# Kernel tuning notes

Measured on AMD Instinct MI355X. Metric: run time of the kernel, lower is better.

The kernel has to match this reference:

```python
import jax, jax.numpy as jnp
import numpy as np

N = 8_388_608        # cohort size (2^23)
T_MAX = 1_000_000    # distinct time values -> ~8 ties per unique time


def setup_inputs() -> dict:
    key = jax.random.key(0)
    k1, k2, k3 = jax.random.split(key, 3)
    x = jax.random.normal(k1, (N,), dtype=jnp.float32)  # risk scores
    times = jax.random.randint(k2, (N,), 0, T_MAX).astype(jnp.float32)
    events = (jax.random.uniform(k3, (N,)) < 0.7).astype(jnp.float32)
    target = jnp.stack([times, events], axis=1)  # [N, 2] = [time, event]
    return {"input": x, "target": target}


def _cox_breslow_sqrt_loss(x, target):
    times = target[:, 0]
    events_all = target[:, 1]
    n = x.shape[0]
    # Sort by descending time (risk set = prefix in this ordering).
    sort_idx = jnp.argsort(-times)
    t = times[sort_idx]
    ev = events_all[sort_idx]
    xs = x[sort_idx]
    # Stable prefix log-sum-exp over the risk set.
    log_cum = jax.lax.cumlogsumexp(xs)
    # end_idx[i] = last index of the tie group containing i (groups are
    # contiguous after sorting). Reverse running-min over positions of
    # group-last elements.
    is_last = jnp.concatenate([t[:-1] != t[1:], jnp.ones((1,), dtype=bool)])
    pos = jnp.where(is_last, jnp.arange(n), n)
    end_idx = jnp.flip(jax.lax.cummin(jnp.flip(pos)))
    # Breslow: -sum(x*ev) + sum_groups logcum[group_end] * (#events in group)
    #        == -sum((x - logcum[end_idx]) * ev)
    loss = -jnp.sum((xs - log_cum[end_idx]) * ev)
    # reduction='mean' -> sqrt(loss / n)
    return jnp.sqrt(loss / n)


def reference(input, target):
    return _cox_breslow_sqrt_loss(input, target)
```

## Files before the change

### kernel.cpp

```cpp
#include <hip/hip_runtime.h>
#include <math.h>

#define TMAX 1000000
#define BINW 4096
#define BINSHIFT 12
#define NBIN 245
#define PADN (NBIN * BINW)
#define TILE 8192
#define NTHR 512
#define CAP 36864
#define CURSOR_STRIDE 16
#define BT_STRIDE 8
#define FIXSCALE 65536.0f
#define INV_FIXSCALE (1.0 / 65536.0)

#define OFF_SCAL     0
#define OFF_DONE     16
#define OFF_CURSOR   64
#define OFF_BINTOT   15744
#define OFF_PAYLOAD  31488
#define MEMSET_BYTES 31424
#define NEED_FULL    ((size_t)OFF_PAYLOAD + (size_t)NBIN * CAP * 4)
#define FB_BINTOT    15744
#define FB_CEXCL     17792
#define FB_BEXP      31488
#define FB_BEV       (FB_BEXP + PADN * 4)
#define NEED_MIN     ((size_t)FB_BEV + PADN * 4)

__device__ __forceinline__ int clamp_tau(float t) {
    int tau = (int)t;
    if (tau < 0) tau = 0;
    if (tau >= TMAX) tau = TMAX - 1;
    return tau;
}

__device__ __forceinline__ unsigned enc_payload(float xv, float tv, float ev_f, int* bin_out) {
    int tau = clamp_tau(tv);
    *bin_out = tau >> BINSHIFT;
    int fine = tau & (BINW - 1);
    float ex = __expf(xv);
    unsigned bb = __float_as_uint(ex);
    bb = (bb + 0x7FFFu + ((bb >> 16) & 1u)) >> 16;
    unsigned ev = (ev_f != 0.0f) ? 1u : 0u;
    return (bb << 16) | ((unsigned)fine << 1) | ev;
}

__device__ __forceinline__ float dec_exp(unsigned p) {
    return __uint_as_float((p >> 16) << 16);
}

__device__ __forceinline__ void hist1(unsigned long long* hist, unsigned p) {
    float ex = dec_exp(p);
    unsigned fx = __float2uint_rn(ex * FIXSCALE);
    unsigned long long add = ((unsigned long long)(p & 1u) << 48) | (unsigned long long)fx;
    atomicAdd(&hist[(p >> 1) & (BINW - 1)], add);
}

__device__ __forceinline__ void hist4(unsigned long long* hist, uint4 pv) {
    hist1(hist, pv.x); hist1(hist, pv.y); hist1(hist, pv.z); hist1(hist, pv.w);
}

__global__ __launch_bounds__(NTHR, 8) void k_scatter(const float* __restrict__ x,
                                                     const float* __restrict__ tgt,
                                                     unsigned* __restrict__ cursor,
                                                     unsigned* __restrict__ payload,
                                                     double* __restrict__ bintot,
                                                     double* __restrict__ evx_out, int n) {
    __shared__ unsigned cnt[256];
    __shared__ unsigned lpre[256];
    __shared__ unsigned pay_lds[TILE];
    __shared__ unsigned char binof2[TILE / 2];
    __shared__ unsigned wtot_s[8];
    __shared__ double wpart[8];
    const int t = threadIdx.x;
    const int lane = t & 63;
    const int wv = t >> 6;
    if (t < 256) cnt[t] = 0;
    __syncthreads();

    const int tile0 = blockIdx.x * TILE;
    const int tilecount = min(TILE, n - tile0);
    unsigned pay[16], meta[16];
    double evx = 0.0;

    if (tilecount == TILE) {
        const float4* x4 = (const float4*)x;
        const float4* t4 = (const float4*)tgt;
        const int g0 = blockIdx.x * (TILE / 4);
#pragma unroll
        for (int j = 0; j < 4; ++j) {
            const int g = g0 + j * NTHR + t;
            float4 xv = x4[g];
            float4 ta = t4[2 * g];
            float4 tb = t4[2 * g + 1];
            float xs[4] = {xv.x, xv.y, xv.z, xv.w};
            float ts[4] = {ta.x, ta.z, tb.x, tb.z};
            float es[4] = {ta.y, ta.w, tb.y, tb.w};
#pragma unroll
            for (int e = 0; e < 4; ++e) {
                int bin;
                unsigned p = enc_payload(xs[e], ts[e], es[e], &bin);
                unsigned r = atomicAdd(&cnt[bin], 1u);
                pay[4 * j + e] = p;
                meta[4 * j + e] = ((unsigned)bin << 13) | r;
                if (p & 1) evx += (double)xs[e];
            }
        }
    } else {
        const float2* tg2 = (const float2*)tgt;
#pragma unroll
        for (int j = 0; j < 16; ++j) {
            int idx = tile0 + j * NTHR + t;
            if (idx < n) {
                float xv = x[idx];
                float2 te = tg2[idx];
                int bin;
                unsigned p = enc_payload(xv, te.x, te.y, &bin);
                unsigned r = atomicAdd(&cnt[bin], 1u);
                pay[j] = p;
                meta[j] = ((unsigned)bin << 13) | r;
                if (p & 1) evx += (double)xv;
            } else {
                meta[j] = 0xFFFFFFFFu;
            }
        }
    }
    __syncthreads();

    const unsigned c = (t < 256) ? cnt[t] : 0u;
    unsigned pfx = c;
#pragma unroll
    for (int d = 1; d < 64; d <<= 1) {
        unsigned u = __shfl_up(pfx, d);
        if (lane >= d) pfx += u;
    }
    if (lane == 63) wtot_s[wv] = pfx;
    __syncthreads();
    unsigned wbase = 0;
    if (t < 256) {
        for (int w = 0; w < wv; ++w) wbase += wtot_s[w];
    }
    const unsigned excl = (t < 256) ? (wbase + pfx - c) : 0u;
    if (t < 256) lpre[t] = excl;

    if (t < NBIN && c) cnt[t] = atomicAdd(&cursor[t * CURSOR_STRIDE], c);

    if (t < NBIN && c) {
        for (unsigned j = (excl + 1) >> 1; 2 * j < excl + c; ++j)
            binof2[j] = (unsigned char)t;
    }
    __syncthreads();

#pragma unroll
    for (int j = 0; j < 16; ++j) {
        if (meta[j] != 0xFFFFFFFFu) {
            unsigned bin = meta[j] >> 13;
            pay_lds[lpre[bin] + (meta[j] & 0x1FFFu)] = pay[j];
        }
    }
    __syncthreads();

    if (t < NBIN && c) {
        float s = 0.0f;
        for (unsigned k = excl; k < excl + c; ++k) s += dec_exp(pay_lds[k]);
        unsafeAtomicAdd(&bintot[t * BT_STRIDE], (double)s);
    }

    for (int k = t; k < tilecount; k += NTHR) {
        unsigned b = binof2[(unsigned)k >> 1];
        if (t & 1) {
            while ((unsigned)k >= lpre[b + 1]) ++b;
        }
        unsigned pos = cnt[b] + ((unsigned)k - lpre[b]);
        if (pos < CAP) payload[(size_t)b * CAP + pos] = pay_lds[k];
    }

#pragma unroll
    for (int d = 32; d > 0; d >>= 1) {
        double u = __shfl_down(evx, d);
        if (lane + d < 64) evx += u;
    }
    if (lane == 0) wpart[wv] = evx;
    __syncthreads();
    if (t == 0) {
        double s = 0.0;
        for (int w = 0; w < 8; ++w) s += wpart[w];
        atomicAdd(evx_out, s);
    }
}

__global__ __launch_bounds__(1024) void k_fused(const unsigned* __restrict__ payload,
                                                const unsigned* __restrict__ cursor,
                                                const double* __restrict__ bintot,
                                                double* __restrict__ scal,
                                                unsigned* __restrict__ done,
                                                float* __restrict__ out, int n) {
    __shared__ unsigned long long hist[BINW];
    __shared__ double wsumA[16];
    __shared__ double wsum[16];
    __shared__ double bcast;
    const int b = blockIdx.x;
    const int t = threadIdx.x;
    const int lane = t & 63;
    const int wv = t >> 6;

#pragma unroll
    for (int j = 0; j < BINW / 1024; ++j) hist[t + j * 1024] = 0ull;
    __syncthreads();

    unsigned cnt = cursor[b * CURSOR_STRIDE];
    if (cnt > CAP) cnt = CAP;
    const unsigned* seg = payload + (size_t)b * CAP;
    const uint4* seg4 = (const uint4*)seg;
    const unsigned n4 = cnt >> 2;
    unsigned i = t;
    for (; i + 1024 < n4; i += 2048) {
        uint4 a = seg4[i];
        uint4 c4 = seg4[i + 1024];
        hist4(hist, a);
        hist4(hist, c4);
    }
    for (; i < n4; i += 1024) hist4(hist, seg4[i]);
    for (unsigned k = (n4 << 2) + t; k < cnt; k += 1024) hist1(hist, seg[k]);
    __syncthreads();

    double ce = 0.0;
    for (int idx = b + 1 + t; idx < NBIN; idx += 1024) ce += bintot[idx * BT_STRIDE];
#pragma unroll
    for (int d = 32; d > 0; d >>= 1) {
        double u = __shfl_down(ce, d);
        if (lane + d < 64) ce += u;
    }
    if (lane == 0) wsumA[wv] = ce;
    __syncthreads();
    if (t == 0) {
        double s = 0.0;
        for (int w = 0; w < 16; ++w) s += wsumA[w];
        bcast = s;
    }
    __syncthreads();
    const double cexcl = bcast;

    const int tb = t * 4;
    double vex[4];
    unsigned vcnt[4];
    double segtot = 0.0;
#pragma unroll
    for (int j = 0; j < 4; ++j) {
        unsigned long long h = hist[tb + j];
        vex[j] = (double)(h & 0xFFFFFFFFFFFFull) * INV_FIXSCALE;
        vcnt[j] = (unsigned)(h >> 48);
        segtot += vex[j];
    }
    double isuf = segtot;
#pragma unroll
    for (int d = 1; d < 64; d <<= 1) {
        double u = __shfl_down(isuf, d);
        if (lane + d < 64) isuf += u;
    }
    if (lane == 0) wsum[wv] = isuf;
    __syncthreads();
    double wexcl = 0.0;
    for (int w = wv + 1; w < 16; ++w) wexcl += wsum[w];

    double run = cexcl + wexcl + (isuf - segtot);
    double local = 0.0;
#pragma unroll
    for (int j = 3; j >= 0; --j) {
        run += vex[j];
        if (vcnt[j]) local += (double)vcnt[j] * log(run);
    }

#pragma unroll
    for (int d = 32; d > 0; d >>= 1) {
        double u = __shfl_down(local, d);
        if (lane + d < 64) local += u;
    }
    if (lane == 0) wsumA[wv] = local;
    __syncthreads();
    if (t == 0) {
        double s = 0.0;
        for (int w = 0; w < 16; ++w) s += wsumA[w];
        unsafeAtomicAdd(&scal[1], s);
        __threadfence();
        unsigned tk = atomicAdd(done, 1u);
        if (tk == NBIN - 1) {
            double ld = unsafeAtomicAdd(&scal[1], 0.0);
            double loss = ld - scal[0];
            if (loss < 0.0) loss = 0.0;
            out[0] = (float)sqrt(loss / (double)n);
        }
    }
}

__global__ void k_accum(const float* __restrict__ x, const float* __restrict__ tgt,
                        float* __restrict__ bexp, float* __restrict__ bev,
                        double* __restrict__ evx_out, int ngroups) {
    double local = 0.0;
    const int nt = gridDim.x * blockDim.x;
    const int tid = blockIdx.x * blockDim.x + threadIdx.x;
    const float4* x4 = (const float4*)x;
    const float4* t4 = (const float4*)tgt;
    for (int g = tid; g < ngroups; g += nt) {
        float4 xv = x4[g];
        float4 ta = t4[2 * g];
        float4 tb = t4[2 * g + 1];
        float xs[4] = {xv.x, xv.y, xv.z, xv.w};
        float ts[4] = {ta.x, ta.z, tb.x, tb.z};
        float es[4] = {ta.y, ta.w, tb.y, tb.w};
#pragma unroll
        for (int j = 0; j < 4; ++j) {
            int tau = clamp_tau(ts[j]);
            unsafeAtomicAdd(&bexp[tau], __expf(xs[j]));
            if (es[j] != 0.0f) unsafeAtomicAdd(&bev[tau], es[j]);
            local += (double)(es[j] * xs[j]);
        }
    }
    __shared__ double sm[256];
    sm[threadIdx.x] = local;
    __syncthreads();
    for (int s = 128; s > 0; s >>= 1) {
        if (threadIdx.x < s) sm[threadIdx.x] += sm[threadIdx.x + s];
        __syncthreads();
    }
    if (threadIdx.x == 0) atomicAdd(evx_out, sm[0]);
}

__global__ void k_chunksum(const float* __restrict__ bexp, double* __restrict__ bintot) {
    const int b = blockIdx.x;
    double local = 0.0;
    for (int i = b * BINW + (int)threadIdx.x; i < (b + 1) * BINW; i += (int)blockDim.x)
        local += (double)bexp[i];
    __shared__ double sm[256];
    sm[threadIdx.x] = local;
    __syncthreads();
    for (int s = 128; s > 0; s >>= 1) {
        if (threadIdx.x < s) sm[threadIdx.x] += sm[threadIdx.x + s];
        __syncthreads();
    }
    if (threadIdx.x == 0) bintot[b] = sm[0];
}

__global__ __launch_bounds__(256) void k_scanbins(const double* __restrict__ bintot,
                                                  double* __restrict__ cexcl) {
    __shared__ double sm[256];
    const int t = threadIdx.x;
    sm[t] = (t < NBIN) ? bintot[t] : 0.0;
    __syncthreads();
    for (int d = 1; d < 256; d <<= 1) {
        double v = (t + d < 256) ? sm[t + d] : 0.0;
        __syncthreads();
        sm[t] += v;
        __syncthreads();
    }
    double e = (t + 1 < 256) ? sm[t + 1] : 0.0;
    __syncthreads();
    cexcl[t] = e;
}

__global__ __launch_bounds__(256) void k_logdot_g(const float* __restrict__ bexp,
                                                  const float* __restrict__ bev,
                                                  const double* __restrict__ cexcl,
                                                  double* __restrict__ logdot) {
    const int b = blockIdx.x;
    const int t = threadIdx.x;
    const float4* e4 = (const float4*)(bexp + b * BINW + t * 16);
    const float4* v4 = (const float4*)(bev + b * BINW + t * 16);
    float ve[16], vv[16];
#pragma unroll
    for (int q = 0; q < 4; ++q) {
        float4 a = e4[q], bb = v4[q];
        ve[4 * q] = a.x; ve[4 * q + 1] = a.y; ve[4 * q + 2] = a.z; ve[4 * q + 3] = a.w;
        vv[4 * q] = bb.x; vv[4 * q + 1] = bb.y; vv[4 * q + 2] = bb.z; vv[4 * q + 3] = bb.w;
    }
    double segtot = 0.0;
#pragma unroll
    for (int j = 0; j < 16; ++j) segtot += (double)ve[j];
    __shared__ double sm[256];
    sm[t] = segtot;
    __syncthreads();
    for (int d = 1; d < 256; d <<= 1) {
        double v = (t + d < 256) ? sm[t + d] : 0.0;
        __syncthreads();
        sm[t] += v;
        __syncthreads();
    }
    double excl = (t < 255) ? sm[t + 1] : 0.0;
    double run = cexcl[b] + excl;
    double local = 0.0;
#pragma unroll
    for (int j = 15; j >= 0; --j) {
        run += (double)ve[j];
        if (vv[j] > 0.0f) local += (double)vv[j] * log(run);
    }
    __syncthreads();
    sm[t] = local;
    __syncthreads();
    for (int s = 128; s > 0; s >>= 1) {
        if (t < s) sm[t] += sm[t + s];
        __syncthreads();
    }
    if (t == 0) atomicAdd(logdot, sm[0]);
}

__global__ void k_final(const double* __restrict__ scal, float* __restrict__ out, int n) {
    if (threadIdx.x == 0 && blockIdx.x == 0) {
        double loss = scal[1] - scal[0];
        if (loss < 0.0) loss = 0.0;
        out[0] = (float)sqrt(loss / (double)n);
    }
}

extern "C" void kernel_launch(void* const* d_in, const int* in_sizes, int n_in,
                              void* d_out, int out_size, void* d_ws, size_t ws_size,
                              hipStream_t stream) {
    const float* x = (const float*)d_in[0];
    const float* tgt = (const float*)d_in[1];
    float* out = (float*)d_out;
    int n = in_sizes[0];

    char* ws = (char*)d_ws;
    double* scal = (double*)(ws + OFF_SCAL);
    unsigned* done = (unsigned*)(ws + OFF_DONE);
    unsigned* cursor = (unsigned*)(ws + OFF_CURSOR);
    double* bintot = (double*)(ws + OFF_BINTOT);
    unsigned* payload = (unsigned*)(ws + OFF_PAYLOAD);

    if (ws_size >= NEED_FULL) {
        hipMemsetAsync(ws, 0, MEMSET_BYTES, stream);
        const int nblk = (n + TILE - 1) / TILE;
        k_scatter<<<nblk, NTHR, 0, stream>>>(x, tgt, cursor, payload, bintot, scal, n);
        k_fused<<<NBIN, 1024, 0, stream>>>(payload, cursor, bintot, scal, done, out, n);
    } else if (ws_size >= NEED_MIN) {
        float* bexp = (float*)(ws + FB_BEXP);
        float* bev = (float*)(ws + FB_BEV);
        double* bintotF = (double*)(ws + FB_BINTOT);
        double* cexclF = (double*)(ws + FB_CEXCL);
        hipMemsetAsync(ws, 0, NEED_MIN, stream);
        k_accum<<<2048, 256, 0, stream>>>(x, tgt, bexp, bev, scal, n / 4);
        k_chunksum<<<NBIN, 256, 0, stream>>>(bexp, bintotF);
        k_scanbins<<<1, 256, 0, stream>>>(bintotF, cexclF);
        k_logdot_g<<<NBIN, 256, 0, stream>>>(bexp, bev, cexclF, scal + 1);
        k_final<<<1, 1, 0, stream>>>(scal, out, n);
    }
}
```

Baseline: 164.9 us.

## Replace bin scatter plus LDS histogram with direct global 64-bit atomic histogram

Removes the two-pass scheme that scattered packed payloads into per-bin global segments and then built per-bin histograms in LDS. Each element now does a 64-bit atomicAdd straight into a global fine-grained histogram of about 8 MB, and a float atomic into a per-block LDS bin-total array. The consumer kernel just reads its histogram slice. This drops the payload write and re-read traffic and the local sort logic. In exchange it adds a larger memset, 8M scattered global atomics with contention on about 1M addresses, and float rather than double accumulation of the per-block bin sums.

```diff
diff --git a/kernel.cpp b/kernel.cpp
--- a/kernel.cpp
+++ b/kernel.cpp
@@ -6,21 +6,14 @@
 #define BINSHIFT 12
 #define NBIN 245
 #define PADN (NBIN * BINW)
-#define TILE 8192
-#define NTHR 512
-#define CAP 36864
-#define CURSOR_STRIDE 16
-#define BT_STRIDE 8
 #define FIXSCALE 65536.0f
 #define INV_FIXSCALE (1.0 / 65536.0)
 
 #define OFF_SCAL     0
 #define OFF_DONE     16
-#define OFF_CURSOR   64
-#define OFF_BINTOT   15744
-#define OFF_PAYLOAD  31488
-#define MEMSET_BYTES 31424
-#define NEED_FULL    ((size_t)OFF_PAYLOAD + (size_t)NBIN * CAP * 4)
+#define OFF_BINTOT   64
+#define OFF_HIST     2048
+#define NEED_HIST    ((size_t)OFF_HIST + (size_t)PADN * 8)
 #define FB_BINTOT    15744
 #define FB_CEXCL     17792
 #define FB_BEXP      31488
@@ -34,145 +27,60 @@
     return tau;
 }
 
-__device__ __forceinline__ unsigned enc_payload(float xv, float tv, float ev_f, int* bin_out) {
-    int tau = clamp_tau(tv);
-    *bin_out = tau >> BINSHIFT;
-    int fine = tau & (BINW - 1);
-    float ex = __expf(xv);
-    unsigned bb = __float_as_uint(ex);
-    bb = (bb + 0x7FFFu + ((bb >> 16) & 1u)) >> 16;
-    unsigned ev = (ev_f != 0.0f) ? 1u : 0u;
-    return (bb << 16) | ((unsigned)fine << 1) | ev;
-}
-
-__device__ __forceinline__ float dec_exp(unsigned p) {
-    return __uint_as_float((p >> 16) << 16);
-}
-
-__device__ __forceinline__ void hist1(unsigned long long* hist, unsigned p) {
-    float ex = dec_exp(p);
-    unsigned fx = __float2uint_rn(ex * FIXSCALE);
-    unsigned long long add = ((unsigned long long)(p & 1u) << 48) | (unsigned long long)fx;
-    atomicAdd(&hist[(p >> 1) & (BINW - 1)], add);
-}
-
-__device__ __forceinline__ void hist4(unsigned long long* hist, uint4 pv) {
-    hist1(hist, pv.x); hist1(hist, pv.y); hist1(hist, pv.z); hist1(hist, pv.w);
-}
-
-__global__ __launch_bounds__(NTHR, 8) void k_scatter(const float* __restrict__ x,
-                                                     const float* __restrict__ tgt,
-                                                     unsigned* __restrict__ cursor,
-                                                     unsigned* __restrict__ payload,
-                                                     double* __restrict__ bintot,
-                                                     double* __restrict__ evx_out, int n) {
-    __shared__ unsigned cnt[256];
-    __shared__ unsigned lpre[256];
-    __shared__ unsigned pay_lds[TILE];
-    __shared__ unsigned char binof2[TILE / 2];
-    __shared__ unsigned wtot_s[8];
-    __shared__ double wpart[8];
+__global__ __launch_bounds__(256) void k_hist(const float* __restrict__ x,
+                                              const float* __restrict__ tgt,
+                                              unsigned long long* __restrict__ hist,
+                                              double* __restrict__ bintot,
+                                              double* __restrict__ scal, int n) {
+    __shared__ float bsum[NBIN];
+    __shared__ double wpart[4];
     const int t = threadIdx.x;
     const int lane = t & 63;
     const int wv = t >> 6;
-    if (t < 256) cnt[t] = 0;
-    __syncthreads();
-
-    const int tile0 = blockIdx.x * TILE;
-    const int tilecount = min(TILE, n - tile0);
-    unsigned pay[16], meta[16];
+    for (int i = t; i < NBIN; i += 256) bsum[i] = 0.0f;
+    __syncthreads();
+
     double evx = 0.0;
-
-    if (tilecount == TILE) {
-        const float4* x4 = (const float4*)x;
-        const float4* t4 = (const float4*)tgt;
-        const int g0 = blockIdx.x * (TILE / 4);
+    const int nth = gridDim.x * 256;
+    const int tid = blockIdx.x * 256 + t;
+    const int ngroups = n >> 2;
+    const float4* x4 = (const float4*)x;
+    const float4* t4 = (const float4*)tgt;
+    for (int g = tid; g < ngroups; g += nth) {
+        float4 xv = x4[g];
+        float4 ta = t4[2 * g];
+        float4 tb = t4[2 * g + 1];
+        float xs[4] = {xv.x, xv.y, xv.z, xv.w};
+        float ts[4] = {ta.x, ta.z, tb.x, tb.z};
+        float es[4] = {ta.y, ta.w, tb.y, tb.w};
 #pragma unroll
         for (int j = 0; j < 4; ++j) {
-            const int g = g0 + j * NTHR + t;
-            float4 xv = x4[g];
-            float4 ta = t4[2 * g];
-            float4 tb = t4[2 * g + 1];
-            float xs[4] = {xv.x, xv.y, xv.z, xv.w};
-            float ts[4] = {ta.x, ta.z, tb.x, tb.z};
-            float es[4] = {ta.y, ta.w, tb.y, tb.w};
-#pragma unroll
-            for (int e = 0; e < 4; ++e) {
-                int bin;
-                unsigned p = enc_payload(xs[e], ts[e], es[e], &bin);
-                unsigned r = atomicAdd(&cnt[bin], 1u);
-                pay[4 * j + e] = p;
-                meta[4 * j + e] = ((unsigned)bin << 13) | r;
-                if (p & 1) evx += (double)xs[e];
-            }
+            int tau = clamp_tau(ts[j]);
+            float ex = __expf(xs[j]);
+            unsigned fx = __float2uint_rn(ex * FIXSCALE);
+            unsigned long long ev = (es[j] != 0.0f) ? 1ull : 0ull;
+            atomicAdd(&hist[tau], (ev << 48) | (unsigned long long)fx);
+            atomicAdd(&bsum[tau >> BINSHIFT], (float)fx * (1.0f / FIXSCALE));
+            if (ev) evx += (double)xs[j];
         }
-    } else {
-        const float2* tg2 = (const float2*)tgt;
-#pragma unroll
-        for (int j = 0; j < 16; ++j) {
-            int idx = tile0 + j * NTHR + t;
-            if (idx < n) {
-                float xv = x[idx];
-                float2 te = tg2[idx];
-                int bin;
-                unsigned p = enc_payload(xv, te.x, te.y, &bin);
-                unsigned r = atomicAdd(&cnt[bin], 1u);
-                pay[j] = p;
-                meta[j] = ((unsigned)bin << 13) | r;
-                if (p & 1) evx += (double)xv;
-            } else {
-                meta[j] = 0xFFFFFFFFu;
-            }
-        }
-    }
-    __syncthreads();
-
-    const unsigned c = (t < 256) ? cnt[t] : 0u;
-    unsigned pfx = c;
-#pragma unroll
-    for (int d = 1; d < 64; d <<= 1) {
-        unsigned u = __shfl_up(pfx, d);
-        if (lane >= d) pfx += u;
-    }
-    if (lane == 63) wtot_s[wv] = pfx;
-    __syncthreads();
-    unsigned wbase = 0;
-    if (t < 256) {
-        for (int w = 0; w < wv; ++w) wbase += wtot_s[w];
-    }
-    const unsigned excl = (t < 256) ? (wbase + pfx - c) : 0u;
-    if (t < 256) lpre[t] = excl;
-
-    if (t < NBIN && c) cnt[t] = atomicAdd(&cursor[t * CURSOR_STRIDE], c);
-
-    if (t < NBIN && c) {
-        for (unsigned j = (excl + 1) >> 1; 2 * j < excl + c; ++j)
-            binof2[j] = (unsigned char)t;
-    }
-    __syncthreads();
-
-#pragma unroll
-    for (int j = 0; j < 16; ++j) {
-        if (meta[j] != 0xFFFFFFFFu) {
-            unsigned bin = meta[j] >> 13;
-            pay_lds[lpre[bin] + (meta[j] & 0x1FFFu)] = pay[j];
-        }
-    }
-    __syncthreads();
-
-    if (t < NBIN && c) {
-        float s = 0.0f;
-        for (unsigned k = excl; k < excl + c; ++k) s += dec_exp(pay_lds[k]);
-        unsafeAtomicAdd(&bintot[t * BT_STRIDE], (double)s);
-    }
-
-    for (int k = t; k < tilecount; k += NTHR) {
-        unsigned b = binof2[(unsigned)k >> 1];
-        if (t & 1) {
-            while ((unsigned)k >= lpre[b + 1]) ++b;
-        }
-        unsigned pos = cnt[b] + ((unsigned)k - lpre[b]);
-        if (pos < CAP) payload[(size_t)b * CAP + pos] = pay_lds[k];
+    }
+    const float2* tg2 = (const float2*)tgt;
+    for (int idx = (ngroups << 2) + tid; idx < n; idx += nth) {
+        float xv = x[idx];
+        float2 te = tg2[idx];
+        int tau = clamp_tau(te.x);
+        float ex = __expf(xv);
+        unsigned fx = __float2uint_rn(ex * FIXSCALE);
+        unsigned long long ev = (te.y != 0.0f) ? 1ull : 0ull;
+        atomicAdd(&hist[tau], (ev << 48) | (unsigned long long)fx);
+        atomicAdd(&bsum[tau >> BINSHIFT], (float)fx * (1.0f / FIXSCALE));
+        if (ev) evx += (double)xv;
+    }
+    __syncthreads();
+
+    for (int i = t; i < NBIN; i += 256) {
+        float s = bsum[i];
+        if (s != 0.0f) unsafeAtomicAdd(&bintot[i], (double)s);
     }
 
 #pragma unroll
@@ -183,19 +91,16 @@
     if (lane == 0) wpart[wv] = evx;
     __syncthreads();
     if (t == 0) {
-        double s = 0.0;
-        for (int w = 0; w < 8; ++w) s += wpart[w];
-        atomicAdd(evx_out, s);
-    }
-}
-
-__global__ __launch_bounds__(1024) void k_fused(const unsigned* __restrict__ payload,
-                                                const unsigned* __restrict__ cursor,
-                                                const double* __restrict__ bintot,
-                                                double* __restrict__ scal,
-                                                unsigned* __restrict__ done,
-                                                float* __restrict__ out, int n) {
-    __shared__ unsigned long long hist[BINW];
+        double s = wpart[0] + wpart[1] + wpart[2] + wpart[3];
+        unsafeAtomicAdd(&scal[0], s);
+    }
+}
+
+__global__ __launch_bounds__(1024) void k_fused2(const unsigned long long* __restrict__ hist,
+                                                 const double* __restrict__ bintot,
+                                                 double* __restrict__ scal,
+                                                 unsigned* __restrict__ done,
+                                                 float* __restrict__ out, int n) {
     __shared__ double wsumA[16];
     __shared__ double wsum[16];
     __shared__ double bcast;
@@ -204,28 +109,12 @@
     const int lane = t & 63;
     const int wv = t >> 6;
 
-#pragma unroll
-    for (int j = 0; j < BINW / 1024; ++j) hist[t + j * 1024] = 0ull;
-    __syncthreads();
-
-    unsigned cnt = cursor[b * CURSOR_STRIDE];
-    if (cnt > CAP) cnt = CAP;
-    const unsigned* seg = payload + (size_t)b * CAP;
-    const uint4* seg4 = (const uint4*)seg;
-    const unsigned n4 = cnt >> 2;
-    unsigned i = t;
-    for (; i + 1024 < n4; i += 2048) {
-        uint4 a = seg4[i];
-        uint4 c4 = seg4[i + 1024];
-        hist4(hist, a);
-        hist4(hist, c4);
-    }
-    for (; i < n4; i += 1024) hist4(hist, seg4[i]);
-    for (unsigned k = (n4 << 2) + t; k < cnt; k += 1024) hist1(hist, seg[k]);
-    __syncthreads();
+    const unsigned long long* hb = hist + (size_t)b * BINW + t * 4;
+    unsigned long long h[4];
+    h[0] = hb[0]; h[1] = hb[1]; h[2] = hb[2]; h[3] = hb[3];
 
     double ce = 0.0;
-    for (int idx = b + 1 + t; idx < NBIN; idx += 1024) ce += bintot[idx * BT_STRIDE];
+    for (int idx = b + 1 + t; idx < NBIN; idx += 1024) ce += bintot[idx];
 #pragma unroll
     for (int d = 32; d > 0; d >>= 1) {
         double u = __shfl_down(ce, d);
@@ -241,15 +130,13 @@
     __syncthreads();
     const double cexcl = bcast;
 
-    const int tb = t * 4;
     double vex[4];
     unsigned vcnt[4];
     double segtot = 0.0;
 #pragma unroll
     for (int j = 0; j < 4; ++j) {
-        unsigned long long h = hist[tb + j];
-        vex[j] = (double)(h & 0xFFFFFFFFFFFFull) * INV_FIXSCALE;
-        vcnt[j] = (unsigned)(h >> 48);
+        vex[j] = (double)(h[j] & 0xFFFFFFFFFFFFull) * INV_FIXSCALE;
+        vcnt[j] = (unsigned)(h[j] >> 48);
         segtot += vex[j];
     }
     double isuf = segtot;
@@ -418,20 +305,18 @@
     const float* tgt = (const float*)d_in[1];
     float* out = (float*)d_out;
     int n = in_sizes[0];
-
     char* ws = (char*)d_ws;
-    double* scal = (double*)(ws + OFF_SCAL);
-    unsigned* done = (unsigned*)(ws + OFF_DONE);
-    unsigned* cursor = (unsigned*)(ws + OFF_CURSOR);
-    double* bintot = (double*)(ws + OFF_BINTOT);
-    unsigned* payload = (unsigned*)(ws + OFF_PAYLOAD);
-
-    if (ws_size >= NEED_FULL) {
-        hipMemsetAsync(ws, 0, MEMSET_BYTES, stream);
-        const int nblk = (n + TILE - 1) / TILE;
-        k_scatter<<<nblk, NTHR, 0, stream>>>(x, tgt, cursor, payload, bintot, scal, n);
-        k_fused<<<NBIN, 1024, 0, stream>>>(payload, cursor, bintot, scal, done, out, n);
+
+    if (ws_size >= NEED_HIST) {
+        double* scal = (double*)(ws + OFF_SCAL);
+        unsigned* done = (unsigned*)(ws + OFF_DONE);
+        double* bintot = (double*)(ws + OFF_BINTOT);
+        unsigned long long* hist = (unsigned long long*)(ws + OFF_HIST);
+        hipMemsetAsync(ws, 0, NEED_HIST, stream);
+        k_hist<<<1024, 256, 0, stream>>>(x, tgt, hist, bintot, scal, n);
+        k_fused2<<<NBIN, 1024, 0, stream>>>(hist, bintot, scal, done, out, n);
     } else if (ws_size >= NEED_MIN) {
+        double* scal = (double*)(ws + OFF_SCAL);
         float* bexp = (float*)(ws + FB_BEXP);
         float* bev = (float*)(ws + FB_BEV);
         double* bintotF = (double*)(ws + FB_BINTOT);
```

Result: slower. 485.6 us (+194.5%).

## Replace atomic-cursor bin scatter with tile-contiguous writes and per-tile offset table

Applied to the files above, without the earlier changes.

The scatter kernel no longer reserves space per bin with global atomic cursors and scatters each bin's run into a per-bin segment. Each tile now writes its locally bin-sorted payload contiguously with coalesced uint4 stores, and records its 256 bin start offsets in a small ushort table. The per-bin gather kernel walks all tiles, reading each tile's short run for its bin (two tiles per wave at a time) into the LDS histogram. This removes global atomics, the scattered write pattern and the CAP overflow limit. In exchange the gather now makes many small, partly filled reads of roughly 30 elements per tile per bin.

```diff
diff --git a/kernel.cpp b/kernel.cpp
--- a/kernel.cpp
+++ b/kernel.cpp
@@ -8,19 +8,15 @@
 #define PADN (NBIN * BINW)
 #define TILE 8192
 #define NTHR 512
-#define CAP 36864
-#define CURSOR_STRIDE 16
 #define BT_STRIDE 8
 #define FIXSCALE 65536.0f
 #define INV_FIXSCALE (1.0 / 65536.0)
 
 #define OFF_SCAL     0
 #define OFF_DONE     16
-#define OFF_CURSOR   64
-#define OFF_BINTOT   15744
-#define OFF_PAYLOAD  31488
-#define MEMSET_BYTES 31424
-#define NEED_FULL    ((size_t)OFF_PAYLOAD + (size_t)NBIN * CAP * 4)
+#define OFF_BINTOT   64
+#define OFF_LPTAB    15744
+#define MEMSET_BYTES 15744
 #define FB_BINTOT    15744
 #define FB_CEXCL     17792
 #define FB_BEXP      31488
@@ -56,20 +52,15 @@
     atomicAdd(&hist[(p >> 1) & (BINW - 1)], add);
 }
 
-__device__ __forceinline__ void hist4(unsigned long long* hist, uint4 pv) {
-    hist1(hist, pv.x); hist1(hist, pv.y); hist1(hist, pv.z); hist1(hist, pv.w);
-}
-
-__global__ __launch_bounds__(NTHR, 8) void k_scatter(const float* __restrict__ x,
-                                                     const float* __restrict__ tgt,
-                                                     unsigned* __restrict__ cursor,
-                                                     unsigned* __restrict__ payload,
-                                                     double* __restrict__ bintot,
-                                                     double* __restrict__ evx_out, int n) {
+__global__ __launch_bounds__(NTHR, 8) void k_scat2(const float* __restrict__ x,
+                                                   const float* __restrict__ tgt,
+                                                   unsigned short* __restrict__ lptab,
+                                                   unsigned* __restrict__ payload,
+                                                   double* __restrict__ bintot,
+                                                   double* __restrict__ evx_out, int n) {
     __shared__ unsigned cnt[256];
     __shared__ unsigned lpre[256];
     __shared__ unsigned pay_lds[TILE];
-    __shared__ unsigned char binof2[TILE / 2];
     __shared__ unsigned wtot_s[8];
     __shared__ double wpart[8];
     const int t = threadIdx.x;
@@ -141,13 +132,9 @@
         for (int w = 0; w < wv; ++w) wbase += wtot_s[w];
     }
     const unsigned excl = (t < 256) ? (wbase + pfx - c) : 0u;
-    if (t < 256) lpre[t] = excl;
-
-    if (t < NBIN && c) cnt[t] = atomicAdd(&cursor[t * CURSOR_STRIDE], c);
-
-    if (t < NBIN && c) {
-        for (unsigned j = (excl + 1) >> 1; 2 * j < excl + c; ++j)
-            binof2[j] = (unsigned char)t;
+    if (t < 256) {
+        lpre[t] = excl;
+        lptab[(size_t)blockIdx.x * 256 + t] = (unsigned short)excl;
     }
     __syncthreads();
 
@@ -166,13 +153,14 @@
         unsafeAtomicAdd(&bintot[t * BT_STRIDE], (double)s);
     }
 
-    for (int k = t; k < tilecount; k += NTHR) {
-        unsigned b = binof2[(unsigned)k >> 1];
-        if (t & 1) {
-            while ((unsigned)k >= lpre[b + 1]) ++b;
-        }
-        unsigned pos = cnt[b] + ((unsigned)k - lpre[b]);
-        if (pos < CAP) payload[(size_t)b * CAP + pos] = pay_lds[k];
+    if (tilecount == TILE) {
+        const uint4* s4 = (const uint4*)pay_lds;
+        uint4* d4 = (uint4*)(payload + (size_t)blockIdx.x * TILE);
+#pragma unroll
+        for (int j = 0; j < 4; ++j) d4[j * NTHR + t] = s4[j * NTHR + t];
+    } else {
+        for (int k = t; k < tilecount; k += NTHR)
+            payload[(size_t)blockIdx.x * TILE + k] = pay_lds[k];
     }
 
 #pragma unroll
@@ -189,12 +177,12 @@
     }
 }
 
-__global__ __launch_bounds__(1024) void k_fused(const unsigned* __restrict__ payload,
-                                                const unsigned* __restrict__ cursor,
-                                                const double* __restrict__ bintot,
-                                                double* __restrict__ scal,
-                                                unsigned* __restrict__ done,
-                                                float* __restrict__ out, int n) {
+__global__ __launch_bounds__(1024) void k_gather(const unsigned* __restrict__ payload,
+                                                 const unsigned short* __restrict__ lptab,
+                                                 const double* __restrict__ bintot,
+                                                 double* __restrict__ scal,
+                                                 unsigned* __restrict__ done,
+                                                 float* __restrict__ out, int n, int ntiles) {
     __shared__ unsigned long long hist[BINW];
     __shared__ double wsumA[16];
     __shared__ double wsum[16];
@@ -208,20 +196,30 @@
     for (int j = 0; j < BINW / 1024; ++j) hist[t + j * 1024] = 0ull;
     __syncthreads();
 
-    unsigned cnt = cursor[b * CURSOR_STRIDE];
-    if (cnt > CAP) cnt = CAP;
-    const unsigned* seg = payload + (size_t)b * CAP;
-    const uint4* seg4 = (const uint4*)seg;
-    const unsigned n4 = cnt >> 2;
-    unsigned i = t;
-    for (; i + 1024 < n4; i += 2048) {
-        uint4 a = seg4[i];
-        uint4 c4 = seg4[i + 1024];
-        hist4(hist, a);
-        hist4(hist, c4);
-    }
-    for (; i < n4; i += 1024) hist4(hist, seg4[i]);
-    for (unsigned k = (n4 << 2) + t; k < cnt; k += 1024) hist1(hist, seg[k]);
+    for (int tau = wv; tau < ntiles; tau += 32) {
+        const int tau2 = tau + 16;
+        const unsigned short* lp0 = lptab + (size_t)tau * 256 + b;
+        unsigned s0 = lp0[0], e0 = lp0[1];
+        unsigned s1 = 0, e1 = 0;
+        const bool have2 = (tau2 < ntiles);
+        if (have2) {
+            const unsigned short* lp1 = lptab + (size_t)tau2 * 256 + b;
+            s1 = lp1[0]; e1 = lp1[1];
+        }
+        const unsigned k0 = s0 + lane, k1 = s1 + lane;
+        const bool v0 = (k0 < e0);
+        const bool v1 = have2 && (k1 < e1);
+        unsigned p0 = 0, p1 = 0;
+        if (v0) p0 = payload[(size_t)tau * TILE + k0];
+        if (v1) p1 = payload[(size_t)tau2 * TILE + k1];
+        if (v0) hist1(hist, p0);
+        if (v1) hist1(hist, p1);
+        for (unsigned k = k0 + 64; k < e0; k += 64)
+            hist1(hist, payload[(size_t)tau * TILE + k]);
+        if (have2)
+            for (unsigned k = k1 + 64; k < e1; k += 64)
+                hist1(hist, payload[(size_t)tau2 * TILE + k]);
+    }
     __syncthreads();
 
     double ce = 0.0;
@@ -418,20 +416,24 @@
     const float* tgt = (const float*)d_in[1];
     float* out = (float*)d_out;
     int n = in_sizes[0];
-
     char* ws = (char*)d_ws;
-    double* scal = (double*)(ws + OFF_SCAL);
-    unsigned* done = (unsigned*)(ws + OFF_DONE);
-    unsigned* cursor = (unsigned*)(ws + OFF_CURSOR);
-    double* bintot = (double*)(ws + OFF_BINTOT);
-    unsigned* payload = (unsigned*)(ws + OFF_PAYLOAD);
-
-    if (ws_size >= NEED_FULL) {
+
+    const size_t ntiles = (size_t)(n + TILE - 1) / TILE;
+    const size_t off_pay = (size_t)OFF_LPTAB + ntiles * 512;
+    const size_t need2 = off_pay + ntiles * (size_t)TILE * 4;
+
+    if (ws_size >= need2 && n >= 4) {
+        double* scal = (double*)(ws + OFF_SCAL);
+        unsigned* done = (unsigned*)(ws + OFF_DONE);
+        double* bintot = (double*)(ws + OFF_BINTOT);
+        unsigned short* lptab = (unsigned short*)(ws + OFF_LPTAB);
+        unsigned* payload = (unsigned*)(ws + off_pay);
         hipMemsetAsync(ws, 0, MEMSET_BYTES, stream);
-        const int nblk = (n + TILE - 1) / TILE;
-        k_scatter<<<nblk, NTHR, 0, stream>>>(x, tgt, cursor, payload, bintot, scal, n);
-        k_fused<<<NBIN, 1024, 0, stream>>>(payload, cursor, bintot, scal, done, out, n);
+        k_scat2<<<(int)ntiles, NTHR, 0, stream>>>(x, tgt, lptab, payload, bintot, scal, n);
+        k_gather<<<NBIN, 1024, 0, stream>>>(payload, lptab, bintot, scal, done, out, n,
+                                            (int)ntiles);
     } else if (ws_size >= NEED_MIN) {
+        double* scal = (double*)(ws + OFF_SCAL);
         float* bexp = (float*)(ws + FB_BEXP);
         float* bev = (float*)(ws + FB_BEV);
         double* bintotF = (double*)(ws + FB_BINTOT);
```

New measurement: 174.6 us. 1.06x slower.
